# Kernel tuning notes

Measured on AMD Instinct MI355X. Metric: run time of the kernel, lower is better.

The kernel has to match this reference:

```python
import jax, jax.numpy as jnp
import numpy as np

# Model hyperparameters (Mamba(dim=256, expand=1, d_state=16, bimamba_type='v2'))
D_MODEL = 256      # dim; expand=1 -> d_inner = D_MODEL
D_STATE = 16
DT_RANK = 16       # ceil(256/16)
D_CONV = 4
BATCH = 2
SEQ = 4096         # H*W = 64*64


def _ln(x, g, b, eps=1e-5):
    m = jnp.mean(x, axis=-1, keepdims=True)
    v = jnp.mean((x - m) ** 2, axis=-1, keepdims=True)
    return (x - m) * jax.lax.rsqrt(v + eps) * g + b


def _causal_dwconv(x, w, b):
    # x: [B, L, d], w: [d, 1, K] (depthwise), causal padding K-1 on the left
    xt = jnp.transpose(x, (0, 2, 1))  # [B, d, L]
    y = jax.lax.conv_general_dilated(
        xt, w, window_strides=(1,), padding=[(w.shape[-1] - 1, 0)],
        dimension_numbers=('NCH', 'OIH', 'NCH'), feature_group_count=xt.shape[1])
    return jnp.transpose(y + b[None, :, None], (0, 2, 1))


def _selective_scan(u, dt, Bm, Cm, A, D, z):
    # u, dt, z: [B, L, d]; Bm, Cm: [B, L, N]; A: [d, N]; D: [d]
    def step(h, inp):
        dt_t, B_t, C_t, u_t = inp            # [B,d], [B,N], [B,N], [B,d]
        h = h * jnp.exp(dt_t[:, :, None] * A) + (dt_t * u_t)[:, :, None] * B_t[:, None, :]
        y = jnp.einsum('bdn,bn->bd', h, C_t)
        return h, y

    h0 = jnp.zeros((u.shape[0], u.shape[2], A.shape[1]), u.dtype)
    xs = (jnp.transpose(dt, (1, 0, 2)), jnp.transpose(Bm, (1, 0, 2)),
          jnp.transpose(Cm, (1, 0, 2)), jnp.transpose(u, (1, 0, 2)))
    _, ys = jax.lax.scan(step, h0, xs)       # ys: [L, B, d]
    y = jnp.transpose(ys, (1, 0, 2)) + u * D
    return y * jax.nn.silu(z)                # SiLU(z) gating (done inside mamba_inner_fn)


def _mamba_dir(xin, z, conv_w, conv_b, xproj_w, dtproj_w, dtproj_b, A_log, D):
    u = jax.nn.silu(_causal_dwconv(xin, conv_w, conv_b))
    dbl = u @ xproj_w.T                       # [B, L, dt_rank + 2*N]
    dt = dbl[..., :DT_RANK]
    Bm = dbl[..., DT_RANK:DT_RANK + D_STATE]
    Cm = dbl[..., DT_RANK + D_STATE:]
    dt = jax.nn.softplus(dt @ dtproj_w.T + dtproj_b)
    return _selective_scan(u, dt, Bm, Cm, -jnp.exp(A_log), D, z)


def setup_inputs() -> dict:
    key = jax.random.key(0)
    ks = jax.random.split(key, 24)
    d, N, R, K = D_MODEL, D_STATE, DT_RANK, D_CONV
    s = 0.02
    A_log = jnp.log(jnp.tile(jnp.arange(1, N + 1, dtype=jnp.float32)[None, :], (d, 1)))
    return {
        'input': jax.random.normal(ks[0], (BATCH, SEQ, d), jnp.float32),
        'norm_g': jnp.ones((d,), jnp.float32),
        'norm_b': jnp.zeros((d,), jnp.float32),
        'in_proj_w': jax.random.normal(ks[1], (2 * d, d), jnp.float32) * s,
        # forward-direction SSM params
        'conv_w': jax.random.normal(ks[2], (d, 1, K), jnp.float32) * 0.1,
        'conv_b': jnp.zeros((d,), jnp.float32),
        'xproj_w': jax.random.normal(ks[3], (R + 2 * N, d), jnp.float32) * s,
        'dtproj_w': jax.random.normal(ks[4], (d, R), jnp.float32) * 0.1,
        'dtproj_b': jax.random.normal(ks[5], (d,), jnp.float32) * 0.1 - 4.0,
        'A_log': A_log,
        'Dp': jnp.ones((d,), jnp.float32),
        # backward-direction SSM params (bimamba v2)
        'conv_w_b': jax.random.normal(ks[6], (d, 1, K), jnp.float32) * 0.1,
        'conv_b_b': jnp.zeros((d,), jnp.float32),
        'xproj_w_b': jax.random.normal(ks[7], (R + 2 * N, d), jnp.float32) * s,
        'dtproj_w_b': jax.random.normal(ks[8], (d, R), jnp.float32) * 0.1,
        'dtproj_b_b': jax.random.normal(ks[9], (d,), jnp.float32) * 0.1 - 4.0,
        'A_log_b': A_log,
        'Dp_b': jnp.ones((d,), jnp.float32),
        # pre-out_proj norm (use_norm=True) and out projection
        'out_norm_g': jnp.ones((d,), jnp.float32),
        'out_norm_b': jnp.zeros((d,), jnp.float32),
        'out_proj_w': jax.random.normal(ks[10], (d, d), jnp.float32) * s,
        'post_norm_g': jnp.ones((d,), jnp.float32),
        'post_norm_b': jnp.zeros((d,), jnp.float32),
    }


def reference(input, norm_g, norm_b, in_proj_w,
              conv_w, conv_b, xproj_w, dtproj_w, dtproj_b, A_log, Dp,
              conv_w_b, conv_b_b, xproj_w_b, dtproj_w_b, dtproj_b_b, A_log_b, Dp_b,
              out_norm_g, out_norm_b, out_proj_w, post_norm_g, post_norm_b):
    skip = input
    x = _ln(input, norm_g, norm_b)
    xz = x @ in_proj_w.T                      # [B, L, 2d]
    xin, z = jnp.split(xz, 2, axis=-1)
    # forward direction
    y_f = _mamba_dir(xin, z, conv_w, conv_b, xproj_w, dtproj_w, dtproj_b, A_log, Dp)
    # backward direction: flip sequence, run, flip back
    y_b = _mamba_dir(xin[:, ::-1], z[:, ::-1], conv_w_b, conv_b_b, xproj_w_b,
                     dtproj_w_b, dtproj_b_b, A_log_b, Dp_b)[:, ::-1]
    y = (y_f + y_b) * 0.5                     # if_devide_out=True
    y = _ln(y, out_norm_g, out_norm_b)        # use_norm=True
    out = y @ out_proj_w.T
    out = _ln(out, post_norm_g, post_norm_b)
    return out + skip
```

## Files before the change

### kernel.cpp

```cpp
#include <hip/hip_runtime.h>
#include <math.h>

#define DM 256
#define SQ 4096
#define BT 2
#define NS 16
#define NTOK (BT*SQ)
#define NCHK 128
#define CHL (SQ/NCHK)

typedef __attribute__((ext_vector_type(8))) short short8;
typedef __attribute__((ext_vector_type(4))) float f32x4;

__device__ __forceinline__ float sigm_(float x){ return 1.f/(1.f+__expf(-x)); }
__device__ __forceinline__ float silu_(float x){ return x*sigm_(x); }
__device__ __forceinline__ float softplus_(float x){ return (x>20.f)? x : log1pf(__expf(x)); }
__device__ __forceinline__ unsigned short f2bf(float f){
  unsigned int u = __float_as_uint(f);
  unsigned int r = (u + 0x7FFFu + ((u>>16)&1u)) >> 16;
  return (unsigned short)r;
}
__device__ __forceinline__ float bf2f(unsigned short u){
  return __uint_as_float(((unsigned int)u)<<16);
}

__global__ __launch_bounds__(256) void k_lncvt(const float* __restrict__ x,
                                               const float* __restrict__ g, const float* __restrict__ nb,
                                               unsigned short* __restrict__ xl){
  int tok = blockIdx.x*4 + (threadIdx.x>>6);
  int lane = threadIdx.x & 63;
  const float* row = x + (size_t)tok*DM;
  float4 v = *(const float4*)(row + lane*4);
  float s = v.x+v.y+v.z+v.w;
  float ss = v.x*v.x+v.y*v.y+v.z*v.z+v.w*v.w;
  #pragma unroll
  for (int o=32;o>0;o>>=1){ s += __shfl_xor(s,o,64); ss += __shfl_xor(ss,o,64); }
  float m = s*(1.f/DM);
  float r = rsqrtf(ss*(1.f/DM)-m*m+1e-5f);
  float4 gv = *(const float4*)(g + lane*4);
  float4 bv = *(const float4*)(nb + lane*4);
  ushort4 o4;
  o4.x = f2bf((v.x-m)*r*gv.x+bv.x);
  o4.y = f2bf((v.y-m)*r*gv.y+bv.y);
  o4.z = f2bf((v.z-m)*r*gv.z+bv.z);
  o4.w = f2bf((v.w-m)*r*gv.w+bv.w);
  *(ushort4*)(xl + (size_t)tok*DM + lane*4) = o4;
}

__global__ __launch_bounds__(256) void k_wcvt(const float* __restrict__ W, unsigned short* __restrict__ Wb){
  int i = (blockIdx.x*256 + threadIdx.x)*4;
  float4 v = *(const float4*)(W + i);
  ushort4 o4; o4.x=f2bf(v.x); o4.y=f2bf(v.y); o4.z=f2bf(v.z); o4.w=f2bf(v.w);
  *(ushort4*)(Wb + i) = o4;
}

__global__ __launch_bounds__(256) void k_inproj_mfma(
    const unsigned short* __restrict__ xl, const unsigned short* __restrict__ Wb,
    float* __restrict__ xin, unsigned short* __restrict__ zb)
{
  int tid = threadIdx.x;
  int wid = tid >> 6, lane = tid & 63;
  int wm = wid >> 1, wn = wid & 1;
  int row0 = blockIdx.x*128 + wm*64;
  int col0 = blockIdx.y*64 + wn*32;
  int lr = lane & 15;
  int lg = lane >> 4;
  f32x4 acc[4][2];
  #pragma unroll
  for (int m=0;m<4;m++)
    #pragma unroll
    for (int n=0;n<2;n++) acc[m][n] = (f32x4){0.f,0.f,0.f,0.f};

  #pragma unroll
  for (int k0=0;k0<DM;k0+=32){
    short8 a[4], b[2];
    #pragma unroll
    for (int m=0;m<4;m++)
      a[m] = *(const short8*)(xl + (size_t)(row0 + m*16 + lr)*DM + k0 + lg*8);
    #pragma unroll
    for (int n=0;n<2;n++)
      b[n] = *(const short8*)(Wb + (size_t)(col0 + n*16 + lr)*DM + k0 + lg*8);
    #pragma unroll
    for (int m=0;m<4;m++)
      #pragma unroll
      for (int n=0;n<2;n++)
        acc[m][n] = __builtin_amdgcn_mfma_f32_16x16x32_bf16(a[m], b[n], acc[m][n], 0,0,0);
  }
  if (blockIdx.y < 4){
    #pragma unroll
    for (int m=0;m<4;m++)
      #pragma unroll
      for (int n=0;n<2;n++)
        #pragma unroll
        for (int r=0;r<4;r++){
          int rr = row0 + m*16 + lg*4 + r;
          int cc = col0 + n*16 + lr;
          xin[(size_t)rr*DM + cc] = acc[m][n][r];
        }
  } else {
    int cb = col0 - 256;
    #pragma unroll
    for (int m=0;m<4;m++)
      #pragma unroll
      for (int n=0;n<2;n++)
        #pragma unroll
        for (int r=0;r<4;r++){
          int rr = row0 + m*16 + lg*4 + r;
          int cc = cb + n*16 + lr;
          zb[(size_t)rr*DM + cc] = f2bf(acc[m][n][r]);
        }
  }
}

__global__ __launch_bounds__(256) void k_conv(
    const float* __restrict__ xin,
    const float* __restrict__ cw_f, const float* __restrict__ cb_f,
    const float* __restrict__ cw_b, const float* __restrict__ cb_b,
    unsigned short* __restrict__ ufb, unsigned short* __restrict__ ubb)
{
  int d = threadIdx.x;
  int b = blockIdx.y;
  int dir = blockIdx.z;
  int t0 = blockIdx.x*16;
  const float* w  = dir? cw_b : cw_f;
  const float* bi = dir? cb_b : cb_f;
  float w0=w[d*4], w1=w[d*4+1], w2=w[d*4+2], w3=w[d*4+3];
  float bb = bi[d];
  unsigned short* outb = dir? ubb : ufb;
  const float* xbase = xin + (size_t)b*SQ*DM + d;
  float xm3 = (t0-3>=0)? xbase[(size_t)(dir?(SQ-1-(t0-3)):(t0-3))*DM] : 0.f;
  float xm2 = (t0-2>=0)? xbase[(size_t)(dir?(SQ-1-(t0-2)):(t0-2))*DM] : 0.f;
  float xm1 = (t0-1>=0)? xbase[(size_t)(dir?(SQ-1-(t0-1)):(t0-1))*DM] : 0.f;
  for (int i=0;i<16;i++){
    int t = t0+i;
    float xt = xbase[(size_t)(dir?(SQ-1-t):t)*DM];
    float v = silu_(bb + w0*xm3 + w1*xm2 + w2*xm1 + w3*xt);
    outb[((size_t)b*SQ+t)*DM + d] = f2bf(v);
    xm3=xm2; xm2=xm1; xm1=xt;
  }
}

__global__ __launch_bounds__(256) void k_wcat(
    const float* __restrict__ xw_f, const float* __restrict__ xw_b,
    const float* __restrict__ dtw_f, const float* __restrict__ dtw_b,
    unsigned short* __restrict__ Wcatb)
{
  int kc = blockIdx.x*64;
  int dir = blockIdx.y;
  const float* xw  = dir? xw_b : xw_f;
  const float* dtw = dir? dtw_b : dtw_f;
  int d = threadIdx.x;
  float dw[16];
  #pragma unroll
  for (int r=0;r<16;r++) dw[r] = dtw[d*16+r];
  unsigned short* Wd = Wcatb + (size_t)dir*320*DM + (size_t)d*DM + kc;
  for (int kk=0;kk<64;kk++){
    float acc = 0.f;
    #pragma unroll
    for (int r=0;r<16;r++) acc += dw[r]*xw[r*DM + kc + kk];
    Wd[kk] = f2bf(acc);
  }
  if (d < 64){
    unsigned short* Wr = Wcatb + (size_t)dir*320*DM + (size_t)(256+d)*DM + kc;
    if (d < 32){
      const float* src = xw + (size_t)(16+d)*DM + kc;
      for (int kk=0;kk<64;kk++) Wr[kk] = f2bf(src[kk]);
    } else {
      for (int kk=0;kk<64;kk++) Wr[kk] = 0;
    }
  }
}

__global__ __launch_bounds__(256) void k_xproj_mfma(
    const unsigned short* __restrict__ ufb, const unsigned short* __restrict__ ubb,
    const unsigned short* __restrict__ Wcatb,
    const float* __restrict__ dtbias_f, const float* __restrict__ dtbias_b,
    unsigned short* __restrict__ dt16f, unsigned short* __restrict__ dt16b,
    float* __restrict__ bmf, float* __restrict__ cmf,
    float* __restrict__ bmb, float* __restrict__ cmb)
{
  int dir = blockIdx.z;
  const unsigned short* u  = dir? ubb : ufb;
  const unsigned short* Wc = Wcatb + (size_t)dir*320*DM;
  const float* dbi = dir? dtbias_b : dtbias_f;
  unsigned short* dt = dir? dt16b : dt16f;
  float* bm = dir? bmb : bmf;
  float* cm = dir? cmb : cmf;
  int tid = threadIdx.x;
  int wid = tid >> 6, lane = tid & 63;
  int wm = wid >> 1, wn = wid & 1;
  int row0 = blockIdx.x*128 + wm*64;
  int col0 = blockIdx.y*64 + wn*32;
  int lr = lane & 15, lg = lane >> 4;
  f32x4 acc[4][2];
  #pragma unroll
  for (int m=0;m<4;m++)
    #pragma unroll
    for (int n=0;n<2;n++) acc[m][n] = (f32x4){0.f,0.f,0.f,0.f};
  #pragma unroll
  for (int k0=0;k0<DM;k0+=32){
    short8 a[4], b[2];
    #pragma unroll
    for (int m=0;m<4;m++)
      a[m] = *(const short8*)(u + (size_t)(row0 + m*16 + lr)*DM + k0 + lg*8);
    #pragma unroll
    for (int n=0;n<2;n++)
      b[n] = *(const short8*)(Wc + (size_t)(col0 + n*16 + lr)*DM + k0 + lg*8);
    #pragma unroll
    for (int m=0;m<4;m++)
      #pragma unroll
      for (int n=0;n<2;n++)
        acc[m][n] = __builtin_amdgcn_mfma_f32_16x16x32_bf16(a[m], b[n], acc[m][n], 0,0,0);
  }
  if (blockIdx.y < 4){
    #pragma unroll
    for (int n=0;n<2;n++){
      int cc = col0 + n*16 + lr;
      float bias = dbi[cc];
      #pragma unroll
      for (int m=0;m<4;m++)
        #pragma unroll
        for (int r=0;r<4;r++){
          int rr = row0 + m*16 + lg*4 + r;
          dt[(size_t)rr*DM + cc] = f2bf(softplus_(acc[m][n][r] + bias));
        }
    }
  } else if (wn == 0){
    #pragma unroll
    for (int n=0;n<2;n++){
      float* outp = n ? cm : bm;
      #pragma unroll
      for (int m=0;m<4;m++)
        #pragma unroll
        for (int r=0;r<4;r++){
          int rr = row0 + m*16 + lg*4 + r;
          outp[(size_t)rr*NS + lr] = acc[m][n][r];
        }
    }
  }
}

__global__ __launch_bounds__(256) void k_scan1(
    const unsigned short* __restrict__ dtf, const unsigned short* __restrict__ dtb,
    const unsigned short* __restrict__ ufb, const unsigned short* __restrict__ ubb,
    const float* __restrict__ bmf, const float* __restrict__ bmb,
    const float* __restrict__ alog_f, const float* __restrict__ alog_b,
    float* __restrict__ apf, float* __restrict__ hsf,
    float* __restrict__ apb, float* __restrict__ hsb)
{
  int c = blockIdx.x, b = blockIdx.y, dir = blockIdx.z;
  const unsigned short* dt = dir? dtb : dtf;
  const unsigned short* u  = dir? ubb : ufb;
  const float* bmp= dir? bmb : bmf;
  const float* al = dir? alog_b : alog_f;
  float* ap = dir? apb : apf;
  float* hs = dir? hsb : hsf;
  int d = threadIdx.x;
  __shared__ float sB[CHL*NS];
  for (int i=threadIdx.x;i<CHL*NS;i+=256) sB[i] = bmp[((size_t)b*SQ + c*CHL)*NS + i];
  float A[NS];
  #pragma unroll
  for (int n=0;n<NS;n++) A[n] = -__expf(al[d*NS+n]);
  float h[NS] = {};
  float dts = 0.f;
  __syncthreads();
  for (int t=0;t<CHL;t++){
    size_t idx = ((size_t)b*SQ + c*CHL + t)*DM + d;
    float dtv = bf2f(dt[idx]);
    float uv  = bf2f(u[idx]);
    float du  = dtv*uv;
    dts += dtv;
    #pragma unroll
    for (int n=0;n<NS;n++) h[n] = h[n]*__expf(dtv*A[n]) + du*sB[t*NS+n];
  }
  size_t o = (((size_t)b*NCHK + c)*DM + d)*NS;
  #pragma unroll
  for (int n=0;n<NS;n++){ hs[o+n] = h[n]; ap[o+n] = __expf(A[n]*dts); }
}

__global__ __launch_bounds__(64) void k_scan2(
    float* __restrict__ apf, float* __restrict__ hsf,
    float* __restrict__ apb, float* __restrict__ hsb)
{
  int gid = blockIdx.x*64 + threadIdx.x;
  int dir = gid >> 13;
  int rem = gid & 8191;
  int b   = rem >> 12;
  int dn  = rem & 4095;
  const float* ap = dir? apb : apf;
  float* hs = dir? hsb : hsf;
  size_t base = (size_t)b*NCHK*4096 + dn;
  float h = 0.f;
  for (int c=0;c<NCHK;c++){
    size_t idx = base + (size_t)c*4096;
    float a = ap[idx];
    float v = hs[idx];
    hs[idx] = h;
    h = h*a + v;
  }
}

__global__ __launch_bounds__(256) void k_scan3(
    const unsigned short* __restrict__ dtf, const unsigned short* __restrict__ dtb,
    const unsigned short* __restrict__ ufb, const unsigned short* __restrict__ ubb,
    const float* __restrict__ bmf, const float* __restrict__ bmb,
    const float* __restrict__ cmf, const float* __restrict__ cmb,
    const float* __restrict__ alf, const float* __restrict__ alb,
    const float* __restrict__ Df, const float* __restrict__ Db,
    const unsigned short* __restrict__ zb,
    const float* __restrict__ hsf, const float* __restrict__ hsb,
    float* __restrict__ yf, float* __restrict__ yb)
{
  int c = blockIdx.x, b = blockIdx.y;
  int dir = blockIdx.z;
  const unsigned short* dt = dir? dtb : dtf;
  const unsigned short* u  = dir? ubb : ufb;
  const float* bmp= dir? bmb : bmf;
  const float* cmp= dir? cmb : cmf;
  const float* al = dir? alb : alf;
  const float* Dv = dir? Db  : Df;
  const float* hs = dir? hsb : hsf;
  float* yout = dir? yb : yf;
  int d = threadIdx.x;
  __shared__ float sB[CHL*NS];
  __shared__ float sC[CHL*NS];
  for (int i=threadIdx.x;i<CHL*NS;i+=256){
    sB[i] = bmp[((size_t)b*SQ + c*CHL)*NS + i];
    sC[i] = cmp[((size_t)b*SQ + c*CHL)*NS + i];
  }
  float A[NS], h[NS];
  size_t o = (((size_t)b*NCHK + c)*DM + d)*NS;
  #pragma unroll
  for (int n=0;n<NS;n++){ A[n] = -__expf(al[d*NS+n]); h[n] = hs[o+n]; }
  float Dd = Dv[d];
  __syncthreads();
  for (int t=0;t<CHL;t++){
    int gt = c*CHL + t;
    size_t idx = ((size_t)b*SQ + gt)*DM + d;
    float dtv = bf2f(dt[idx]);
    float uv  = bf2f(u[idx]);
    float du  = dtv*uv;
    float y = 0.f;
    #pragma unroll
    for (int n=0;n<NS;n++){
      h[n] = h[n]*__expf(dtv*A[n]) + du*sB[t*NS+n];
      y += h[n]*sC[t*NS+n];
    }
    y += uv*Dd;
    int torig = dir ? (SQ-1-gt) : gt;
    size_t oidx = ((size_t)b*SQ + torig)*DM + d;
    float zv = bf2f(zb[oidx]);
    yout[oidx] = y * (zv * sigm_(zv));
  }
}

__global__ __launch_bounds__(256) void k_ycvt(const float* __restrict__ yf, const float* __restrict__ yb,
                                              const float* __restrict__ og, const float* __restrict__ ob,
                                              unsigned short* __restrict__ ybf){
  int tok = blockIdx.x*4 + (threadIdx.x>>6);
  int lane = threadIdx.x & 63;
  size_t base = (size_t)tok*DM;
  float4 vf = *(const float4*)(yf + base + lane*4);
  float4 vb = *(const float4*)(yb + base + lane*4);
  float4 v; v.x=0.5f*(vf.x+vb.x); v.y=0.5f*(vf.y+vb.y); v.z=0.5f*(vf.z+vb.z); v.w=0.5f*(vf.w+vb.w);
  float s = v.x+v.y+v.z+v.w;
  float ss = v.x*v.x+v.y*v.y+v.z*v.z+v.w*v.w;
  #pragma unroll
  for (int o=32;o>0;o>>=1){ s += __shfl_xor(s,o,64); ss += __shfl_xor(ss,o,64); }
  float m = s*(1.f/DM);
  float r = rsqrtf(ss*(1.f/DM)-m*m+1e-5f);
  float4 gv = *(const float4*)(og + lane*4);
  float4 bv = *(const float4*)(ob + lane*4);
  ushort4 o4;
  o4.x = f2bf((v.x-m)*r*gv.x+bv.x);
  o4.y = f2bf((v.y-m)*r*gv.y+bv.y);
  o4.z = f2bf((v.z-m)*r*gv.z+bv.z);
  o4.w = f2bf((v.w-m)*r*gv.w+bv.w);
  *(ushort4*)(ybf + base + lane*4) = o4;
}

#define SOS 266
__global__ __launch_bounds__(256) void k_final_mfma(
    const unsigned short* __restrict__ ybf, const unsigned short* __restrict__ Wb,
    const float* __restrict__ pg, const float* __restrict__ pb,
    const float* __restrict__ skip, float* __restrict__ out)
{
  __shared__ float sOut[32*SOS];
  __shared__ float sm[32], sr[32];
  int tid = threadIdx.x;
  int wid = tid >> 6, lane = tid & 63;
  int lr = lane & 15, lg = lane >> 4;
  int row0 = blockIdx.x*32;
  int col0 = wid*64;
  f32x4 acc[2][4];
  #pragma unroll
  for (int m=0;m<2;m++)
    #pragma unroll
    for (int n=0;n<4;n++) acc[m][n] = (f32x4){0.f,0.f,0.f,0.f};
  #pragma unroll
  for (int k0=0;k0<DM;k0+=32){
    short8 a[2], b[4];
    #pragma unroll
    for (int m=0;m<2;m++)
      a[m] = *(const short8*)(ybf + (size_t)(row0 + m*16 + lr)*DM + k0 + lg*8);
    #pragma unroll
    for (int n=0;n<4;n++)
      b[n] = *(const short8*)(Wb + (size_t)(col0 + n*16 + lr)*DM + k0 + lg*8);
    #pragma unroll
    for (int m=0;m<2;m++)
      #pragma unroll
      for (int n=0;n<4;n++)
        acc[m][n] = __builtin_amdgcn_mfma_f32_16x16x32_bf16(a[m], b[n], acc[m][n], 0,0,0);
  }
  #pragma unroll
  for (int m=0;m<2;m++)
    #pragma unroll
    for (int n=0;n<4;n++)
      #pragma unroll
      for (int r=0;r<4;r++)
        sOut[(m*16 + lg*4 + r)*SOS + col0 + n*16 + lr] = acc[m][n][r];
  __syncthreads();
  for (int j=0;j<8;j++){
    int rrow = wid*8 + j;
    const float* rp = &sOut[rrow*SOS + lane*4];
    float2 v0 = *(const float2*)(rp);
    float2 v1 = *(const float2*)(rp+2);
    float s = v0.x+v0.y+v1.x+v1.y;
    float ss = v0.x*v0.x+v0.y*v0.y+v1.x*v1.x+v1.y*v1.y;
    #pragma unroll
    for (int o=32;o>0;o>>=1){ s += __shfl_xor(s,o,64); ss += __shfl_xor(ss,o,64); }
    if (lane==0){ float m=s*(1.f/DM); sm[rrow]=m; sr[rrow]=rsqrtf(ss*(1.f/DM)-m*m+1e-5f); }
  }
  __syncthreads();
  float gv = pg[tid], bv = pb[tid];
  for (int rrow=0;rrow<32;rrow++){
    int tok = row0 + rrow;
    float v = (sOut[rrow*SOS + tid]-sm[rrow])*sr[rrow]*gv + bv + skip[(size_t)tok*DM + tid];
    out[(size_t)tok*DM + tid] = v;
  }
}

extern "C" void kernel_launch(void* const* d_in, const int* in_sizes, int n_in,
                              void* d_out, int out_size, void* d_ws, size_t ws_size,
                              hipStream_t stream)
{
  const float* input      = (const float*)d_in[0];
  const float* norm_g     = (const float*)d_in[1];
  const float* norm_b     = (const float*)d_in[2];
  const float* in_proj_w  = (const float*)d_in[3];
  const float* conv_w     = (const float*)d_in[4];
  const float* conv_b     = (const float*)d_in[5];
  const float* xproj_w    = (const float*)d_in[6];
  const float* dtproj_w   = (const float*)d_in[7];
  const float* dtproj_b   = (const float*)d_in[8];
  const float* A_log      = (const float*)d_in[9];
  const float* Dp         = (const float*)d_in[10];
  const float* conv_w_b   = (const float*)d_in[11];
  const float* conv_b_b   = (const float*)d_in[12];
  const float* xproj_w_b  = (const float*)d_in[13];
  const float* dtproj_w_b = (const float*)d_in[14];
  const float* dtproj_b_b = (const float*)d_in[15];
  const float* A_log_b    = (const float*)d_in[16];
  const float* Dp_b       = (const float*)d_in[17];
  const float* out_norm_g = (const float*)d_in[18];
  const float* out_norm_b = (const float*)d_in[19];
  const float* out_proj_w = (const float*)d_in[20];
  const float* post_norm_g= (const float*)d_in[21];
  const float* post_norm_b= (const float*)d_in[22];
  float* out = (float*)d_out;

  float* ws = (float*)d_ws;
  const size_t M2 = (size_t)NTOK*DM;
  const size_t SCH = (size_t)BT*NCHK*DM*NS;
  float* xin = ws;
  float* yf  = xin;
  unsigned short* zbuf = (unsigned short*)(ws + M2);
  unsigned short* aux  = (unsigned short*)(ws + M2 + M2/2);
  float* yb = ws + 2*M2;
  unsigned short* dt16f = (unsigned short*)(ws + 3*M2);
  unsigned short* dt16b = dt16f + M2;
  unsigned short* ufb = (unsigned short*)(ws + 4*M2);
  unsigned short* ubb = ufb + M2;
  float* p   = ws + 5*M2;
  float* bmf = p;              p += (size_t)NTOK*NS;
  float* cmf = p;              p += (size_t)NTOK*NS;
  float* bmb = p;              p += (size_t)NTOK*NS;
  float* cmb = p;              p += (size_t)NTOK*NS;
  float* apf = p;              p += SCH;
  float* hsf = p;              p += SCH;
  float* apb = p;              p += SCH;
  float* hsb = p;              p += SCH;
  unsigned short* xlbf = (unsigned short*)apf;
  unsigned short* ybf  = (unsigned short*)apf;

  k_lncvt<<<NTOK/4, 256, 0, stream>>>(input, norm_g, norm_b, xlbf);
  k_wcvt<<<(2*DM*DM)/1024, 256, 0, stream>>>(in_proj_w, aux);
  k_inproj_mfma<<<dim3(NTOK/128, 8, 1), 256, 0, stream>>>(xlbf, aux, xin, zbuf);
  k_conv<<<dim3(SQ/16, BT, 2), 256, 0, stream>>>(xin, conv_w, conv_b, conv_w_b, conv_b_b,
                                                 ufb, ubb);
  k_wcat<<<dim3(4, 2), 256, 0, stream>>>(xproj_w, xproj_w_b, dtproj_w, dtproj_w_b, aux);
  k_xproj_mfma<<<dim3(NTOK/128, 5, 2), 256, 0, stream>>>(ufb, ubb, aux,
                                                         dtproj_b, dtproj_b_b,
                                                         dt16f, dt16b, bmf, cmf, bmb, cmb);
  k_scan1<<<dim3(NCHK, BT, 2), 256, 0, stream>>>(dt16f, dt16b, ufb, ubb, bmf, bmb,
                                                 A_log, A_log_b, apf, hsf, apb, hsb);
  k_scan2<<<256, 64, 0, stream>>>(apf, hsf, apb, hsb);
  k_wcvt<<<(DM*DM)/1024, 256, 0, stream>>>(out_proj_w, aux);
  k_scan3<<<dim3(NCHK, BT, 2), 256, 0, stream>>>(dt16f, dt16b, ufb, ubb, bmf, bmb, cmf, cmb,
                                                 A_log, A_log_b, Dp, Dp_b, zbuf, hsf, hsb,
                                                 yf, yb);
  k_ycvt<<<NTOK/4, 256, 0, stream>>>(yf, yb, out_norm_g, out_norm_b, ybf);
  k_final_mfma<<<NTOK/32, 256, 0, stream>>>(ybf, aux, post_norm_g, post_norm_b, input, out);
}
```

Measured before the change: 160.7 us.

## Fuse prep kernels, merge bidirectional conv, parallelize chunk scan, store y as bf16

Folds the input layernorm, the three weight conversions and the x/dt weight fusion into a single prep launch, which removes several tiny launches. The two conv directions are computed in one kernel that reads xin once, writing the forward output and the flipped backward output together. The inter-chunk scan now stages chunk data in shared memory and splits the 128 chunks across four thread groups with a two-level prefix, giving more parallelism than one serial thread per element. Scan outputs are stored as bf16 to halve the traffic into the y-normalization kernel, at some cost in precision.

Measured after the change: 144.6 us. 1.11x faster.

```diff
diff --git a/kernel.cpp b/kernel.cpp
--- a/kernel.cpp
+++ b/kernel.cpp
@@ -24,34 +24,73 @@
   return __uint_as_float(((unsigned int)u)<<16);
 }
 
-__global__ __launch_bounds__(256) void k_lncvt(const float* __restrict__ x,
-                                               const float* __restrict__ g, const float* __restrict__ nb,
-                                               unsigned short* __restrict__ xl){
-  int tok = blockIdx.x*4 + (threadIdx.x>>6);
-  int lane = threadIdx.x & 63;
-  const float* row = x + (size_t)tok*DM;
-  float4 v = *(const float4*)(row + lane*4);
-  float s = v.x+v.y+v.z+v.w;
-  float ss = v.x*v.x+v.y*v.y+v.z*v.z+v.w*v.w;
-  #pragma unroll
-  for (int o=32;o>0;o>>=1){ s += __shfl_xor(s,o,64); ss += __shfl_xor(ss,o,64); }
-  float m = s*(1.f/DM);
-  float r = rsqrtf(ss*(1.f/DM)-m*m+1e-5f);
-  float4 gv = *(const float4*)(g + lane*4);
-  float4 bv = *(const float4*)(nb + lane*4);
-  ushort4 o4;
-  o4.x = f2bf((v.x-m)*r*gv.x+bv.x);
-  o4.y = f2bf((v.y-m)*r*gv.y+bv.y);
-  o4.z = f2bf((v.z-m)*r*gv.z+bv.z);
-  o4.w = f2bf((v.w-m)*r*gv.w+bv.w);
-  *(ushort4*)(xl + (size_t)tok*DM + lane*4) = o4;
-}
-
-__global__ __launch_bounds__(256) void k_wcvt(const float* __restrict__ W, unsigned short* __restrict__ Wb){
-  int i = (blockIdx.x*256 + threadIdx.x)*4;
-  float4 v = *(const float4*)(W + i);
-  ushort4 o4; o4.x=f2bf(v.x); o4.y=f2bf(v.y); o4.z=f2bf(v.z); o4.w=f2bf(v.w);
-  *(ushort4*)(Wb + i) = o4;
+__global__ __launch_bounds__(256) void k_prep(
+    const float* __restrict__ x, const float* __restrict__ g, const float* __restrict__ nb,
+    unsigned short* __restrict__ xl,
+    const float* __restrict__ Win, unsigned short* __restrict__ Wbin,
+    const float* __restrict__ xw_f, const float* __restrict__ xw_b,
+    const float* __restrict__ dtw_f, const float* __restrict__ dtw_b,
+    unsigned short* __restrict__ Wcatb,
+    const float* __restrict__ Wout, unsigned short* __restrict__ Wbout)
+{
+  int bx = blockIdx.x;
+  int tid = threadIdx.x;
+  if (bx < NTOK/4){
+    int tok = bx*4 + (tid>>6);
+    int lane = tid & 63;
+    const float* row = x + (size_t)tok*DM;
+    float4 v = *(const float4*)(row + lane*4);
+    float s = v.x+v.y+v.z+v.w;
+    float ss = v.x*v.x+v.y*v.y+v.z*v.z+v.w*v.w;
+    #pragma unroll
+    for (int o=32;o>0;o>>=1){ s += __shfl_xor(s,o,64); ss += __shfl_xor(ss,o,64); }
+    float m = s*(1.f/DM);
+    float r = rsqrtf(ss*(1.f/DM)-m*m+1e-5f);
+    float4 gv = *(const float4*)(g + lane*4);
+    float4 bv = *(const float4*)(nb + lane*4);
+    ushort4 o4;
+    o4.x = f2bf((v.x-m)*r*gv.x+bv.x);
+    o4.y = f2bf((v.y-m)*r*gv.y+bv.y);
+    o4.z = f2bf((v.z-m)*r*gv.z+bv.z);
+    o4.w = f2bf((v.w-m)*r*gv.w+bv.w);
+    *(ushort4*)(xl + (size_t)tok*DM + lane*4) = o4;
+  } else if (bx < NTOK/4 + 128){
+    int i = ((bx - NTOK/4)*256 + tid)*4;
+    float4 v = *(const float4*)(Win + i);
+    ushort4 o4; o4.x=f2bf(v.x); o4.y=f2bf(v.y); o4.z=f2bf(v.z); o4.w=f2bf(v.w);
+    *(ushort4*)(Wbin + i) = o4;
+  } else if (bx < NTOK/4 + 136){
+    int idx = bx - (NTOK/4 + 128);
+    int dir = idx >> 2;
+    int kc = (idx & 3)*64;
+    const float* xw  = dir? xw_b : xw_f;
+    const float* dtw = dir? dtw_b : dtw_f;
+    int d = tid;
+    float dw[16];
+    #pragma unroll
+    for (int r=0;r<16;r++) dw[r] = dtw[d*16+r];
+    unsigned short* Wd = Wcatb + (size_t)dir*320*DM + (size_t)d*DM + kc;
+    for (int kk=0;kk<64;kk++){
+      float acc = 0.f;
+      #pragma unroll
+      for (int r=0;r<16;r++) acc += dw[r]*xw[r*DM + kc + kk];
+      Wd[kk] = f2bf(acc);
+    }
+    if (d < 64){
+      unsigned short* Wr = Wcatb + (size_t)dir*320*DM + (size_t)(256+d)*DM + kc;
+      if (d < 32){
+        const float* src = xw + (size_t)(16+d)*DM + kc;
+        for (int kk=0;kk<64;kk++) Wr[kk] = f2bf(src[kk]);
+      } else {
+        for (int kk=0;kk<64;kk++) Wr[kk] = 0;
+      }
+    }
+  } else {
+    int i = ((bx - (NTOK/4 + 136))*256 + tid)*4;
+    float4 v = *(const float4*)(Wout + i);
+    ushort4 o4; o4.x=f2bf(v.x); o4.y=f2bf(v.y); o4.z=f2bf(v.z); o4.w=f2bf(v.w);
+    *(ushort4*)(Wbout + i) = o4;
+  }
 }
 
 __global__ __launch_bounds__(256) void k_inproj_mfma(
@@ -112,7 +151,7 @@
   }
 }
 
-__global__ __launch_bounds__(256) void k_conv(
+__global__ __launch_bounds__(256) void k_conv2(
     const float* __restrict__ xin,
     const float* __restrict__ cw_f, const float* __restrict__ cb_f,
     const float* __restrict__ cw_b, const float* __restrict__ cb_b,
@@ -120,54 +159,27 @@
 {
   int d = threadIdx.x;
   int b = blockIdx.y;
-  int dir = blockIdx.z;
   int t0 = blockIdx.x*16;
-  const float* w  = dir? cw_b : cw_f;
-  const float* bi = dir? cb_b : cb_f;
-  float w0=w[d*4], w1=w[d*4+1], w2=w[d*4+2], w3=w[d*4+3];
-  float bb = bi[d];
-  unsigned short* outb = dir? ubb : ufb;
+  float wf0=cw_f[d*4], wf1=cw_f[d*4+1], wf2=cw_f[d*4+2], wf3=cw_f[d*4+3];
+  float wb0=cw_b[d*4], wb1=cw_b[d*4+1], wb2=cw_b[d*4+2], wb3=cw_b[d*4+3];
+  float bfv = cb_f[d], bbv = cb_b[d];
   const float* xbase = xin + (size_t)b*SQ*DM + d;
-  float xm3 = (t0-3>=0)? xbase[(size_t)(dir?(SQ-1-(t0-3)):(t0-3))*DM] : 0.f;
-  float xm2 = (t0-2>=0)? xbase[(size_t)(dir?(SQ-1-(t0-2)):(t0-2))*DM] : 0.f;
-  float xm1 = (t0-1>=0)? xbase[(size_t)(dir?(SQ-1-(t0-1)):(t0-1))*DM] : 0.f;
+  float r0 = (t0-3>=0)? xbase[(size_t)(t0-3)*DM] : 0.f;
+  float r1 = (t0-2>=0)? xbase[(size_t)(t0-2)*DM] : 0.f;
+  float r2 = (t0-1>=0)? xbase[(size_t)(t0-1)*DM] : 0.f;
+  float r3 = xbase[(size_t)(t0+0)*DM];
+  float r4 = xbase[(size_t)(t0+1)*DM];
+  float r5 = xbase[(size_t)(t0+2)*DM];
+  float r6 = xbase[(size_t)(t0+3)*DM];
   for (int i=0;i<16;i++){
     int t = t0+i;
-    float xt = xbase[(size_t)(dir?(SQ-1-t):t)*DM];
-    float v = silu_(bb + w0*xm3 + w1*xm2 + w2*xm1 + w3*xt);
-    outb[((size_t)b*SQ+t)*DM + d] = f2bf(v);
-    xm3=xm2; xm2=xm1; xm1=xt;
-  }
-}
-
-__global__ __launch_bounds__(256) void k_wcat(
-    const float* __restrict__ xw_f, const float* __restrict__ xw_b,
-    const float* __restrict__ dtw_f, const float* __restrict__ dtw_b,
-    unsigned short* __restrict__ Wcatb)
-{
-  int kc = blockIdx.x*64;
-  int dir = blockIdx.y;
-  const float* xw  = dir? xw_b : xw_f;
-  const float* dtw = dir? dtw_b : dtw_f;
-  int d = threadIdx.x;
-  float dw[16];
-  #pragma unroll
-  for (int r=0;r<16;r++) dw[r] = dtw[d*16+r];
-  unsigned short* Wd = Wcatb + (size_t)dir*320*DM + (size_t)d*DM + kc;
-  for (int kk=0;kk<64;kk++){
-    float acc = 0.f;
-    #pragma unroll
-    for (int r=0;r<16;r++) acc += dw[r]*xw[r*DM + kc + kk];
-    Wd[kk] = f2bf(acc);
-  }
-  if (d < 64){
-    unsigned short* Wr = Wcatb + (size_t)dir*320*DM + (size_t)(256+d)*DM + kc;
-    if (d < 32){
-      const float* src = xw + (size_t)(16+d)*DM + kc;
-      for (int kk=0;kk<64;kk++) Wr[kk] = f2bf(src[kk]);
-    } else {
-      for (int kk=0;kk<64;kk++) Wr[kk] = 0;
-    }
+    float vf = silu_(bfv + wf0*r0 + wf1*r1 + wf2*r2 + wf3*r3);
+    ufb[((size_t)b*SQ+t)*DM + d] = f2bf(vf);
+    float vb = silu_(bbv + wb3*r3 + wb2*r4 + wb1*r5 + wb0*r6);
+    ubb[((size_t)b*SQ+(SQ-1-t))*DM + d] = f2bf(vb);
+    r0=r1; r1=r2; r2=r3; r3=r4; r4=r5; r5=r6;
+    int tn = t+4;
+    r6 = (tn<=SQ-1)? xbase[(size_t)tn*DM] : 0.f;
   }
 }
 
@@ -278,25 +290,45 @@
   for (int n=0;n<NS;n++){ hs[o+n] = h[n]; ap[o+n] = __expf(A[n]*dts); }
 }
 
-__global__ __launch_bounds__(64) void k_scan2(
+__global__ __launch_bounds__(256) void k_scan2(
     float* __restrict__ apf, float* __restrict__ hsf,
     float* __restrict__ apb, float* __restrict__ hsb)
 {
-  int gid = blockIdx.x*64 + threadIdx.x;
-  int dir = gid >> 13;
-  int rem = gid & 8191;
-  int b   = rem >> 12;
-  int dn  = rem & 4095;
+  __shared__ float sa[NCHK][64];
+  __shared__ float sv[NCHK][64];
+  __shared__ float segA[4][64], segV[4][64];
+  int bx = blockIdx.x;
+  int dg = bx & 63, b = (bx>>6)&1, dir = bx>>7;
   const float* ap = dir? apb : apf;
   float* hs = dir? hsb : hsf;
-  size_t base = (size_t)b*NCHK*4096 + dn;
-  float h = 0.f;
-  for (int c=0;c<NCHK;c++){
+  int dn = threadIdx.x & 63;
+  int cg = threadIdx.x >> 6;
+  size_t base = (size_t)b*NCHK*4096 + dg*64 + dn;
+  for (int i=0;i<32;i++){
+    int c = cg*32 + i;
     size_t idx = base + (size_t)c*4096;
-    float a = ap[idx];
-    float v = hs[idx];
-    hs[idx] = h;
-    h = h*a + v;
+    sa[c][dn] = ap[idx];
+    sv[c][dn] = hs[idx];
+  }
+  __syncthreads();
+  float A = 1.f, V = 0.f;
+  for (int i=0;i<32;i++){
+    int c = cg*32 + i;
+    float a = sa[c][dn], v = sv[c][dn];
+    V = a*V + v;
+    A = A*a;
+  }
+  segA[cg][dn] = A; segV[cg][dn] = V;
+  __syncthreads();
+  float pre = 0.f;
+  for (int s=0;s<cg;s++) pre = segA[s][dn]*pre + segV[s][dn];
+  float xv = pre;
+  for (int i=0;i<32;i++){
+    int c = cg*32 + i;
+    size_t idx = base + (size_t)c*4096;
+    hs[idx] = xv;
+    float a = sa[c][dn], v = sv[c][dn];
+    xv = a*xv + v;
   }
 }
 
@@ -309,7 +341,7 @@
     const float* __restrict__ Df, const float* __restrict__ Db,
     const unsigned short* __restrict__ zb,
     const float* __restrict__ hsf, const float* __restrict__ hsb,
-    float* __restrict__ yf, float* __restrict__ yb)
+    unsigned short* __restrict__ yf, unsigned short* __restrict__ yb)
 {
   int c = blockIdx.x, b = blockIdx.y;
   int dir = blockIdx.z;
@@ -320,7 +352,7 @@
   const float* al = dir? alb : alf;
   const float* Dv = dir? Db  : Df;
   const float* hs = dir? hsb : hsf;
-  float* yout = dir? yb : yf;
+  unsigned short* yout = dir? yb : yf;
   int d = threadIdx.x;
   __shared__ float sB[CHL*NS];
   __shared__ float sC[CHL*NS];
@@ -350,19 +382,24 @@
     int torig = dir ? (SQ-1-gt) : gt;
     size_t oidx = ((size_t)b*SQ + torig)*DM + d;
     float zv = bf2f(zb[oidx]);
-    yout[oidx] = y * (zv * sigm_(zv));
-  }
-}
-
-__global__ __launch_bounds__(256) void k_ycvt(const float* __restrict__ yf, const float* __restrict__ yb,
+    yout[oidx] = f2bf(y * (zv * sigm_(zv)));
+  }
+}
+
+__global__ __launch_bounds__(256) void k_ycvt(const unsigned short* __restrict__ yf,
+                                              const unsigned short* __restrict__ yb,
                                               const float* __restrict__ og, const float* __restrict__ ob,
                                               unsigned short* __restrict__ ybf){
   int tok = blockIdx.x*4 + (threadIdx.x>>6);
   int lane = threadIdx.x & 63;
   size_t base = (size_t)tok*DM;
-  float4 vf = *(const float4*)(yf + base + lane*4);
-  float4 vb = *(const float4*)(yb + base + lane*4);
-  float4 v; v.x=0.5f*(vf.x+vb.x); v.y=0.5f*(vf.y+vb.y); v.z=0.5f*(vf.z+vb.z); v.w=0.5f*(vf.w+vb.w);
+  ushort4 hf = *(const ushort4*)(yf + base + lane*4);
+  ushort4 hb = *(const ushort4*)(yb + base + lane*4);
+  float4 v;
+  v.x = 0.5f*(bf2f(hf.x)+bf2f(hb.x));
+  v.y = 0.5f*(bf2f(hf.y)+bf2f(hb.y));
+  v.z = 0.5f*(bf2f(hf.z)+bf2f(hb.z));
+  v.w = 0.5f*(bf2f(hf.w)+bf2f(hb.w));
   float s = v.x+v.y+v.z+v.w;
   float ss = v.x*v.x+v.y*v.y+v.z*v.z+v.w*v.w;
   #pragma unroll
@@ -473,10 +510,13 @@
   const size_t M2 = (size_t)NTOK*DM;
   const size_t SCH = (size_t)BT*NCHK*DM*NS;
   float* xin = ws;
-  float* yf  = xin;
+  unsigned short* y16f = (unsigned short*)ws;
+  unsigned short* y16b = (unsigned short*)ws + M2;
   unsigned short* zbuf = (unsigned short*)(ws + M2);
-  unsigned short* aux  = (unsigned short*)(ws + M2 + M2/2);
-  float* yb = ws + 2*M2;
+  unsigned short* auxw = (unsigned short*)(ws + M2 + M2/2);
+  unsigned short* Wbin  = auxw;
+  unsigned short* Wcatb = auxw + 131072;
+  unsigned short* Wbout = auxw + 131072 + 163840;
   unsigned short* dt16f = (unsigned short*)(ws + 3*M2);
   unsigned short* dt16b = dt16f + M2;
   unsigned short* ufb = (unsigned short*)(ws + 4*M2);
@@ -493,22 +533,22 @@
   unsigned short* xlbf = (unsigned short*)apf;
   unsigned short* ybf  = (unsigned short*)apf;
 
-  k_lncvt<<<NTOK/4, 256, 0, stream>>>(input, norm_g, norm_b, xlbf);
-  k_wcvt<<<(2*DM*DM)/1024, 256, 0, stream>>>(in_proj_w, aux);
-  k_inproj_mfma<<<dim3(NTOK/128, 8, 1), 256, 0, stream>>>(xlbf, aux, xin, zbuf);
-  k_conv<<<dim3(SQ/16, BT, 2), 256, 0, stream>>>(xin, conv_w, conv_b, conv_w_b, conv_b_b,
-                                                 ufb, ubb);
-  k_wcat<<<dim3(4, 2), 256, 0, stream>>>(xproj_w, xproj_w_b, dtproj_w, dtproj_w_b, aux);
-  k_xproj_mfma<<<dim3(NTOK/128, 5, 2), 256, 0, stream>>>(ufb, ubb, aux,
+  k_prep<<<NTOK/4 + 136 + 64, 256, 0, stream>>>(input, norm_g, norm_b, xlbf,
+                                                in_proj_w, Wbin,
+                                                xproj_w, xproj_w_b, dtproj_w, dtproj_w_b, Wcatb,
+                                                out_proj_w, Wbout);
+  k_inproj_mfma<<<dim3(NTOK/128, 8, 1), 256, 0, stream>>>(xlbf, Wbin, xin, zbuf);
+  k_conv2<<<dim3(SQ/16, BT), 256, 0, stream>>>(xin, conv_w, conv_b, conv_w_b, conv_b_b,
+                                               ufb, ubb);
+  k_xproj_mfma<<<dim3(NTOK/128, 5, 2), 256, 0, stream>>>(ufb, ubb, Wcatb,
                                                          dtproj_b, dtproj_b_b,
                                                          dt16f, dt16b, bmf, cmf, bmb, cmb);
   k_scan1<<<dim3(NCHK, BT, 2), 256, 0, stream>>>(dt16f, dt16b, ufb, ubb, bmf, bmb,
                                                  A_log, A_log_b, apf, hsf, apb, hsb);
-  k_scan2<<<256, 64, 0, stream>>>(apf, hsf, apb, hsb);
-  k_wcvt<<<(DM*DM)/1024, 256, 0, stream>>>(out_proj_w, aux);
+  k_scan2<<<256, 256, 0, stream>>>(apf, hsf, apb, hsb);
   k_scan3<<<dim3(NCHK, BT, 2), 256, 0, stream>>>(dt16f, dt16b, ufb, ubb, bmf, bmb, cmf, cmb,
                                                  A_log, A_log_b, Dp, Dp_b, zbuf, hsf, hsb,
-                                                 yf, yb);
-  k_ycvt<<<NTOK/4, 256, 0, stream>>>(yf, yb, out_norm_g, out_norm_b, ybf);
-  k_final_mfma<<<NTOK/32, 256, 0, stream>>>(ybf, aux, post_norm_g, post_norm_b, input, out);
-}
+                                                 y16f, y16b);
+  k_ycvt<<<NTOK/4, 256, 0, stream>>>(y16f, y16b, out_norm_g, out_norm_b, ybf);
+  k_final_mfma<<<NTOK/32, 256, 0, stream>>>(ybf, Wbout, post_norm_g, post_norm_b, input, out);
+}
```
